# Kernel optimization log

Hardware: AMD Instinct MI355X
Metric: run time of the kernel (lower is better)

The kernel has to match this reference:

```python
import jax, jax.numpy as jnp
import numpy as np

B, M, A, NS, T = 256, 16, 4096, 1024, 64
DT = 0.001          # dt
DA = DT             # da == dt
REF_T = 0.004       # refractory period (s)
SYN_DELAY_BINS = 1  # floor(syn_delay / da)
N_NEUR = 500.0      # neurons per population (self.N)
A_GRID = jnp.linspace(0.0, A * DA, A + 1)[:-1]  # (A,) ages since last spike


def _get_plam(input_total, V_old, age, rp, amem, ft):
    # V_old: (B,M,K); input_total: (B,M,1); age broadcasts against (B,M,K)
    V_new = V_old + DA * (rp - V_old) * amem + DA * input_total
    V_new = jnp.where(age < REF_T, 0.0, V_new)
    lam = jnp.where(V_new == 0.0, 1e-8, jnp.exp(V_new - ft))  # firing intensity
    p = lam * DT
    Plam = jnp.where(p >= 0.01, 1.0 - jnp.exp(-p), p)
    return V_new, Plam, lam


def setup_inputs() -> dict:
    key = jax.random.key(0)
    ks = jax.random.split(key, 13)
    return {
        "x": jax.random.normal(ks[0], (B, M), jnp.float32),
        "V_t_old": jax.random.normal(ks[1], (B, M, A), jnp.float32),
        "logS_t_old": jax.random.normal(ks[2], (B, M, A), jnp.float32),
        "sampled_neuron_v": jax.random.normal(ks[3], (B, M, NS), jnp.float32),
        "sampled_neuron_lastfire": jax.random.uniform(ks[4], (B, M, NS), jnp.float32),
        "I_syn": jax.random.uniform(ks[5], (B, M, 1), jnp.float32),
        "amem": jax.random.uniform(ks[6], (M, 1), jnp.float32),
        "asyn": jax.random.uniform(ks[7], (M, 1), jnp.float32),
        "J": jax.random.normal(ks[8], (M, M), jnp.float32),
        "rp": jax.random.uniform(ks[9], (M, 1), jnp.float32),
        "ft": jax.random.uniform(ks[10], (M, 1), jnp.float32),
        "eps": jax.random.uniform(ks[11], (1,), jnp.float32),
        "Z_hist_est": jnp.clip(jax.random.uniform(ks[12], (B, M, A + T), jnp.float32), 1e-5, 1.0),
        "internal_clock": 32,
    }


def reference(x, V_t_old, logS_t_old, sampled_neuron_v, sampled_neuron_lastfire,
              I_syn, amem, asyn, J, rp, ft, eps, Z_hist_est, internal_clock):
    clk = int(internal_clock)
    # ---- synaptic current with exponential decay and delayed pop activity ----
    exp_syn = jnp.exp(-DT * asyn)  # (M,1)
    if clk > SYN_DELAY_BINS:
        Z_t_last = Z_hist_est[:, :, clk + A - SYN_DELAY_BINS - 1:clk + A - SYN_DELAY_BINS]
        I_syn = exp_syn * I_syn + (1.0 - exp_syn) * Z_t_last / DT
    # input_total: (B,M,1)
    input_total = jnp.einsum('bm,mn->bn', I_syn[:, :, 0], J)[:, :, None] + (x * eps)[:, :, None]

    # ---- population activity update ----
    Z_t = Z_hist_est[:, :, clk:clk + A][:, :, ::-1]          # (B,M,A), youngest age first
    Z_t_new = Z_hist_est[:, :, clk + A:clk + A + 1]          # (B,M,1)

    V_t_new, Plam, _ = _get_plam(input_total, V_t_old, A_GRID, rp, amem, ft)

    S_old = jnp.exp(logS_t_old)
    m_t = S_old * Z_t
    Zmacro = jnp.sum(m_t * Plam, axis=2, keepdims=True)
    mess = 1.0 - jnp.sum(m_t, axis=2, keepdims=True)
    v_t = (1.0 - S_old) * m_t
    num = jnp.sum(v_t * Plam, axis=2, keepdims=True)
    den = jnp.sum(v_t, axis=2, keepdims=True)
    lambda_t = jnp.where(den != 0.0, num / jnp.where(den == 0.0, 1.0, den), 0.0)  # nan -> 0
    Z = jnp.clip(Zmacro + lambda_t * mess, 0.0, 1.0)
    A_t = Z / DT
    var = Z / N_NEUR + 0.1 * DT / N_NEUR
    Z_nll = 0.5 * jnp.square(Z_t_new - Z) / var + 0.5 * jnp.log(var) + 0.5 * jnp.log(2.0 * 3.14)

    # ---- sampled-neuron spike likelihood ----
    snv_new, Plam_s, lam_s = _get_plam(input_total, sampled_neuron_v, sampled_neuron_lastfire, rp, amem, ft)
    ltdt = lam_s * DT
    lnPy = jnp.where(ltdt < 0.01, snv_new - ft + jnp.log(DT), jnp.log(Plam_s))
    lnP1_y = -ltdt

    return (A_t, Z, Z_nll, lnPy, lnP1_y, V_t_new, snv_new, I_syn)
```

## Files before the change

kernel.cpp:

```cpp
#include <hip/hip_runtime.h>

#define B_   256
#define M_   16
#define A_   4096
#define NS_  1024
#define T_   64
#define AT_  (A_ + T_)

static constexpr float DTc = 0.001f;
static constexpr float DAc = 0.001f;

static constexpr size_t OFF_AT    = 0;
static constexpr size_t OFF_Z     = 4096;
static constexpr size_t OFF_ZNLL  = 8192;
static constexpr size_t OFF_LNPY  = 12288;
static constexpr size_t OFF_LNP1Y = 12288 + 4194304;
static constexpr size_t OFF_VT    = 12288 + 2ull * 4194304;
static constexpr size_t OFF_SNV   = OFF_VT + 16777216ull;
static constexpr size_t OFF_ISYN  = OFF_SNV + 4194304ull;

__global__ __launch_bounds__(256) void lif_kernel(
    const float* __restrict__ x,
    const float* __restrict__ V_t_old,
    const float* __restrict__ logS_t_old,
    const float* __restrict__ snv_in,
    const float* __restrict__ snlf,
    const float* __restrict__ I_syn,
    const float* __restrict__ amem,
    const float* __restrict__ asyn,
    const float* __restrict__ J,
    const float* __restrict__ rp,
    const float* __restrict__ ft,
    const float* __restrict__ eps,
    const float* __restrict__ Z_hist,
    const int*   __restrict__ clk_ptr,
    float* __restrict__ out)
{
    const int row = blockIdx.x;
    const int b   = row >> 4;
    const int m   = row & 15;
    const int tid = threadIdx.x;

    __shared__ float sh_I[M_];
    __shared__ float sh_inT;
    __shared__ float sh_red[4][4];

    const int clk = *clk_ptr;

    if (tid < M_) {
        float es   = expf(-DTc * asyn[tid]);
        float Iold = I_syn[b * M_ + tid];
        float In   = Iold;
        if (clk > 1) {
            float zl = Z_hist[(size_t)(b * M_ + tid) * AT_ + (clk + A_ - 2)];
            In = es * Iold + (1.0f - es) * zl / DTc;
        }
        sh_I[tid] = In;
    }
    __syncthreads();
    if (tid == 0) {
        float dot = 0.0f;
#pragma unroll
        for (int mm = 0; mm < M_; ++mm) dot += sh_I[mm] * J[mm * M_ + m];
        sh_inT = dot + x[row] * eps[0];
        out[OFF_ISYN + row] = sh_I[m];
    }
    __syncthreads();

    const float a_m  = amem[m];
    const float rp_m = rp[m];
    const float ft_m = ft[m];
    const float inT  = sh_inT;

    const size_t rowA = (size_t)row * A_;
    const size_t rowZ = (size_t)row * AT_;

    float sZm = 0.0f, sM = 0.0f, sNum = 0.0f, sDen = 0.0f;

#pragma unroll
    for (int c = 0; c < 4; ++c) {
        const int a0 = c * 1024 + tid * 4;
        const float4 vo = *reinterpret_cast<const float4*>(V_t_old    + rowA + a0);
        const float4 ls = *reinterpret_cast<const float4*>(logS_t_old + rowA + a0);
        const float vov[4] = {vo.x, vo.y, vo.z, vo.w};
        const float lsv[4] = {ls.x, ls.y, ls.z, ls.w};
        const float* zp = Z_hist + rowZ + (clk + A_ - 1 - a0);
        float vres[4];
#pragma unroll
        for (int k = 0; k < 4; ++k) {
            const int a = a0 + k;
            float V = vov[k] + DAc * (rp_m - vov[k]) * a_m + DAc * inT;
            if (a < 4) V = 0.0f;
            float lam  = (V == 0.0f) ? 1e-8f : expf(V - ft_m);
            float p    = lam * DTc;
            float Plam = (p >= 0.01f) ? (1.0f - expf(-p)) : p;
            float S    = expf(lsv[k]);
            float z    = zp[-k];
            float mt   = S * z;
            sZm += mt * Plam;
            sM  += mt;
            float v = (1.0f - S) * mt;
            sNum += v * Plam;
            sDen += v;
            vres[k] = V;
        }
        *reinterpret_cast<float4*>(out + OFF_VT + rowA + a0) =
            make_float4(vres[0], vres[1], vres[2], vres[3]);
    }

    float vals[4] = {sZm, sM, sNum, sDen};
#pragma unroll
    for (int i = 0; i < 4; ++i) {
        float v = vals[i];
        for (int off = 32; off > 0; off >>= 1) v += __shfl_down(v, off, 64);
        vals[i] = v;
    }
    const int wave = tid >> 6, lane = tid & 63;
    if (lane == 0) {
#pragma unroll
        for (int i = 0; i < 4; ++i) sh_red[wave][i] = vals[i];
    }
    __syncthreads();
    if (tid == 0) {
        float Zm  = sh_red[0][0] + sh_red[1][0] + sh_red[2][0] + sh_red[3][0];
        float sMt = sh_red[0][1] + sh_red[1][1] + sh_red[2][1] + sh_red[3][1];
        float num = sh_red[0][2] + sh_red[1][2] + sh_red[2][2] + sh_red[3][2];
        float den = sh_red[0][3] + sh_red[1][3] + sh_red[2][3] + sh_red[3][3];
        float mess  = 1.0f - sMt;
        float lam_t = (den != 0.0f) ? (num / den) : 0.0f;
        float Z = Zm + lam_t * mess;
        Z = fminf(fmaxf(Z, 0.0f), 1.0f);
        float At  = Z / DTc;
        float var = Z / 500.0f + 0.1f * DTc / 500.0f;
        float ztn = Z_hist[rowZ + clk + A_];
        float d   = ztn - Z;
        float znll = 0.5f * (d * d) / var + 0.5f * logf(var) + 0.5f * logf(2.0f * 3.14f);
        out[OFF_AT   + row] = At;
        out[OFF_Z    + row] = Z;
        out[OFF_ZNLL + row] = znll;
    }

    {
        const size_t rowS = (size_t)row * NS_;
        const int s0 = tid * 4;
        const float4 v4  = *reinterpret_cast<const float4*>(snv_in + rowS + s0);
        const float4 lf4 = *reinterpret_cast<const float4*>(snlf   + rowS + s0);
        const float vv[4] = {v4.x, v4.y, v4.z, v4.w};
        const float lf[4] = {lf4.x, lf4.y, lf4.z, lf4.w};
        float vn[4], py[4], p1[4];
#pragma unroll
        for (int k = 0; k < 4; ++k) {
            float V = vv[k] + DAc * (rp_m - vv[k]) * a_m + DAc * inT;
            if (lf[k] < 0.004f) V = 0.0f;
            float lam  = (V == 0.0f) ? 1e-8f : expf(V - ft_m);
            float ltdt = lam * DTc;
            float Plam = (ltdt >= 0.01f) ? (1.0f - expf(-ltdt)) : ltdt;
            py[k] = (ltdt < 0.01f) ? (V - ft_m + logf(DTc)) : logf(Plam);
            p1[k] = -ltdt;
            vn[k] = V;
        }
        *reinterpret_cast<float4*>(out + OFF_SNV   + rowS + s0) = make_float4(vn[0], vn[1], vn[2], vn[3]);
        *reinterpret_cast<float4*>(out + OFF_LNPY  + rowS + s0) = make_float4(py[0], py[1], py[2], py[3]);
        *reinterpret_cast<float4*>(out + OFF_LNP1Y + rowS + s0) = make_float4(p1[0], p1[1], p1[2], p1[3]);
    }
}

extern "C" void kernel_launch(void* const* d_in, const int* in_sizes, int n_in,
                              void* d_out, int out_size, void* d_ws, size_t ws_size,
                              hipStream_t stream) {
    lif_kernel<<<B_ * M_, 256, 0, stream>>>(
        (const float*)d_in[0],
        (const float*)d_in[1],
        (const float*)d_in[2],
        (const float*)d_in[3],
        (const float*)d_in[4],
        (const float*)d_in[5],
        (const float*)d_in[6],
        (const float*)d_in[7],
        (const float*)d_in[8],
        (const float*)d_in[9],
        (const float*)d_in[10],
        (const float*)d_in[11],
        (const float*)d_in[12],
        (const int*)  d_in[13],
        (float*)d_out);
}
```

Before: 312.0 us.

## Hoist all global loads upfront and compute synaptic input via wave shuffles

All V, logS, Z-history and sampled-neuron loads are issued at the start, before the synaptic-input computation, and scheduling barriers keep them grouped so memory latency overlaps the dot product. The 16-element I_syn·J dot product now runs as a shuffle reduction inside each wavefront, which removes two block-wide __syncthreads and the shared-memory round trip. Z-history loads become reversed float4 loads when clk is aligned, the sampled-neuron work moves ahead of the final block reduction, and launch bounds request 4 blocks per CU. The cost is higher register pressure from holding many float4 values live at once, which could lower occupancy.

```diff
diff --git a/kernel.cpp b/kernel.cpp
--- a/kernel.cpp
+++ b/kernel.cpp
@@ -9,6 +9,7 @@
 
 static constexpr float DTc = 0.001f;
 static constexpr float DAc = 0.001f;
+static constexpr float LOG_DT = -6.907755278982137f;
 
 static constexpr size_t OFF_AT    = 0;
 static constexpr size_t OFF_Z     = 4096;
@@ -19,7 +20,11 @@
 static constexpr size_t OFF_SNV   = OFF_VT + 16777216ull;
 static constexpr size_t OFF_ISYN  = OFF_SNV + 4194304ull;
 
-__global__ __launch_bounds__(256) void lif_kernel(
+static __device__ __forceinline__ float4 ld4(const float* p) {
+    return *reinterpret_cast<const float4*>(p);
+}
+
+__global__ __launch_bounds__(256, 4) void lif_kernel(
     const float* __restrict__ x,
     const float* __restrict__ V_t_old,
     const float* __restrict__ logS_t_old,
@@ -36,116 +41,108 @@
     const int*   __restrict__ clk_ptr,
     float* __restrict__ out)
 {
-    const int row = blockIdx.x;
-    const int b   = row >> 4;
-    const int m   = row & 15;
-    const int tid = threadIdx.x;
-
-    __shared__ float sh_I[M_];
-    __shared__ float sh_inT;
+    const int row  = blockIdx.x;
+    const int b    = row >> 4;
+    const int m    = row & 15;
+    const int tid  = threadIdx.x;
+    const int lane = tid & 63;
+
     __shared__ float sh_red[4][4];
 
-    const int clk = *clk_ptr;
-
-    if (tid < M_) {
-        float es   = expf(-DTc * asyn[tid]);
-        float Iold = I_syn[b * M_ + tid];
-        float In   = Iold;
-        if (clk > 1) {
-            float zl = Z_hist[(size_t)(b * M_ + tid) * AT_ + (clk + A_ - 2)];
-            In = es * Iold + (1.0f - es) * zl / DTc;
-        }
-        sh_I[tid] = In;
-    }
-    __syncthreads();
-    if (tid == 0) {
-        float dot = 0.0f;
-#pragma unroll
-        for (int mm = 0; mm < M_; ++mm) dot += sh_I[mm] * J[mm * M_ + m];
-        sh_inT = dot + x[row] * eps[0];
-        out[OFF_ISYN + row] = sh_I[m];
-    }
-    __syncthreads();
-
+    const size_t rowA = (size_t)row * A_;
+    const size_t rowS = (size_t)row * NS_;
+
+    const int   clk  = *clk_ptr;
+    const float xv   = x[row];
+    const float ev   = eps[0];
     const float a_m  = amem[m];
     const float rp_m = rp[m];
     const float ft_m = ft[m];
-    const float inT  = sh_inT;
-
-    const size_t rowA = (size_t)row * A_;
+
     const size_t rowZ = (size_t)row * AT_;
-
-    float sZm = 0.0f, sM = 0.0f, sNum = 0.0f, sDen = 0.0f;
-
-#pragma unroll
-    for (int c = 0; c < 4; ++c) {
-        const int a0 = c * 1024 + tid * 4;
-        const float4 vo = *reinterpret_cast<const float4*>(V_t_old    + rowA + a0);
-        const float4 ls = *reinterpret_cast<const float4*>(logS_t_old + rowA + a0);
-        const float vov[4] = {vo.x, vo.y, vo.z, vo.w};
-        const float lsv[4] = {ls.x, ls.y, ls.z, ls.w};
-        const float* zp = Z_hist + rowZ + (clk + A_ - 1 - a0);
-        float vres[4];
-#pragma unroll
-        for (int k = 0; k < 4; ++k) {
-            const int a = a0 + k;
-            float V = vov[k] + DAc * (rp_m - vov[k]) * a_m + DAc * inT;
-            if (a < 4) V = 0.0f;
-            float lam  = (V == 0.0f) ? 1e-8f : expf(V - ft_m);
-            float p    = lam * DTc;
-            float Plam = (p >= 0.01f) ? (1.0f - expf(-p)) : p;
-            float S    = expf(lsv[k]);
-            float z    = zp[-k];
-            float mt   = S * z;
-            sZm += mt * Plam;
-            sM  += mt;
-            float v = (1.0f - S) * mt;
-            sNum += v * Plam;
-            sDen += v;
-            vres[k] = V;
-        }
-        *reinterpret_cast<float4*>(out + OFF_VT + rowA + a0) =
-            make_float4(vres[0], vres[1], vres[2], vres[3]);
-    }
-
-    float vals[4] = {sZm, sM, sNum, sDen};
-#pragma unroll
-    for (int i = 0; i < 4; ++i) {
-        float v = vals[i];
-        for (int off = 32; off > 0; off >>= 1) v += __shfl_down(v, off, 64);
-        vals[i] = v;
-    }
-    const int wave = tid >> 6, lane = tid & 63;
-    if (lane == 0) {
-#pragma unroll
-        for (int i = 0; i < 4; ++i) sh_red[wave][i] = vals[i];
-    }
-    __syncthreads();
-    if (tid == 0) {
-        float Zm  = sh_red[0][0] + sh_red[1][0] + sh_red[2][0] + sh_red[3][0];
-        float sMt = sh_red[0][1] + sh_red[1][1] + sh_red[2][1] + sh_red[3][1];
-        float num = sh_red[0][2] + sh_red[1][2] + sh_red[2][2] + sh_red[3][2];
-        float den = sh_red[0][3] + sh_red[1][3] + sh_red[2][3] + sh_red[3][3];
-        float mess  = 1.0f - sMt;
-        float lam_t = (den != 0.0f) ? (num / den) : 0.0f;
-        float Z = Zm + lam_t * mess;
-        Z = fminf(fmaxf(Z, 0.0f), 1.0f);
-        float At  = Z / DTc;
-        float var = Z / 500.0f + 0.1f * DTc / 500.0f;
-        float ztn = Z_hist[rowZ + clk + A_];
-        float d   = ztn - Z;
-        float znll = 0.5f * (d * d) / var + 0.5f * logf(var) + 0.5f * logf(2.0f * 3.14f);
-        out[OFF_AT   + row] = At;
-        out[OFF_Z    + row] = Z;
-        out[OFF_ZNLL + row] = znll;
-    }
+    const float  ztn  = Z_hist[rowZ + clk + A_];
+
+    float asy = 0.0f, Iold = 0.0f, Jv = 0.0f, zl = 0.0f;
+    if (lane < M_) {
+        asy  = asyn[lane];
+        Iold = I_syn[b * M_ + lane];
+        Jv   = J[lane * M_ + m];
+        if (clk > 1) zl = Z_hist[(size_t)(b * M_ + lane) * AT_ + (clk + A_ - 2)];
+    }
+    __builtin_amdgcn_sched_barrier(0);
+
+    const float* pV = V_t_old    + rowA + tid * 4;
+    const float* pS = logS_t_old + rowA + tid * 4;
+    const float4 vA = ld4(pV);          const float4 vB = ld4(pV + 1024);
+    const float4 vC = ld4(pV + 2048);   const float4 vD = ld4(pV + 3072);
+    const float4 sA = ld4(pS);          const float4 sB = ld4(pS + 1024);
+    const float4 sC = ld4(pS + 2048);   const float4 sD = ld4(pS + 3072);
+    const float4 n4  = ld4(snv_in + rowS + tid * 4);
+    const float4 lf4 = ld4(snlf   + rowS + tid * 4);
+
+    const bool  zal = ((clk & 3) == 0);
+    const float* pZ = Z_hist + rowZ + (clk + A_ - 4 - tid * 4);
+    float4 zA, zB, zC, zD;
+    if (zal) {
+        zA = ld4(pZ);          zB = ld4(pZ - 1024);
+        zC = ld4(pZ - 2048);   zD = ld4(pZ - 3072);
+    } else {
+        zA = make_float4(pZ[0], pZ[1], pZ[2], pZ[3]);
+        zB = make_float4(pZ[-1024], pZ[-1023], pZ[-1022], pZ[-1021]);
+        zC = make_float4(pZ[-2048], pZ[-2047], pZ[-2046], pZ[-2045]);
+        zD = make_float4(pZ[-3072], pZ[-3071], pZ[-3070], pZ[-3069]);
+    }
+    __builtin_amdgcn_sched_barrier(0);
+
+    float In = Iold;
+    if (clk > 1 && lane < M_) {
+        const float es = expf(-DTc * asy);
+        In = es * Iold + (1.0f - es) * zl / DTc;
+    }
+    if (tid == m) out[OFF_ISYN + row] = In;
+    float t = (lane < M_) ? In * Jv : 0.0f;
+#pragma unroll
+    for (int off = 8; off > 0; off >>= 1) t += __shfl_xor(t, off, 16);
+    const float inT = __shfl(t, 0, 64) + xv * ev;
+
+    float sZm = 0.0f, sMt = 0.0f, sNum = 0.0f, sDen = 0.0f;
+
+#define CHUNK(cidx, vc, sc, zc)                                                 \
+    do {                                                                        \
+        const int a0 = (cidx) * 1024 + tid * 4;                                 \
+        const float vov[4]  = {vc.x, vc.y, vc.z, vc.w};                         \
+        const float lsv[4]  = {sc.x, sc.y, sc.z, sc.w};                         \
+        const float zrev[4] = {zc.w, zc.z, zc.y, zc.x};                         \
+        float vres[4];                                                          \
+        _Pragma("unroll")                                                       \
+        for (int k = 0; k < 4; ++k) {                                           \
+            const int a = a0 + k;                                               \
+            float V = vov[k] + DAc * (rp_m - vov[k]) * a_m + DAc * inT;         \
+            if (a < 4) V = 0.0f;                               \
+            float lam  = (V == 0.0f) ? 1e-8f : expf(V - ft_m);                  \
+            float p    = lam * DTc;                                             \
+            float Plam = (p >= 0.01f) ? (1.0f - expf(-p)) : p;                  \
+            float S    = expf(lsv[k]);                                          \
+            float mt   = S * zrev[k];                                           \
+            sZm += mt * Plam;                                                   \
+            sMt += mt;                                                          \
+            float v = (1.0f - S) * mt;                                          \
+            sNum += v * Plam;                                                   \
+            sDen += v;                                                          \
+            vres[k] = V;                                                        \
+        }                                                                       \
+        *reinterpret_cast<float4*>(out + OFF_VT + rowA + a0) =                  \
+            make_float4(vres[0], vres[1], vres[2], vres[3]);                    \
+    } while (0)
+
+    CHUNK(0, vA, sA, zA);
+    CHUNK(1, vB, sB, zB);
+    CHUNK(2, vC, sC, zC);
+    CHUNK(3, vD, sD, zD);
+#undef CHUNK
 
     {
-        const size_t rowS = (size_t)row * NS_;
-        const int s0 = tid * 4;
-        const float4 v4  = *reinterpret_cast<const float4*>(snv_in + rowS + s0);
-        const float4 lf4 = *reinterpret_cast<const float4*>(snlf   + rowS + s0);
-        const float vv[4] = {v4.x, v4.y, v4.z, v4.w};
+        const float vv[4] = {n4.x, n4.y, n4.z, n4.w};
         const float lf[4] = {lf4.x, lf4.y, lf4.z, lf4.w};
         float vn[4], py[4], p1[4];
 #pragma unroll
@@ -155,13 +152,45 @@
             float lam  = (V == 0.0f) ? 1e-8f : expf(V - ft_m);
             float ltdt = lam * DTc;
             float Plam = (ltdt >= 0.01f) ? (1.0f - expf(-ltdt)) : ltdt;
-            py[k] = (ltdt < 0.01f) ? (V - ft_m + logf(DTc)) : logf(Plam);
+            py[k] = (ltdt < 0.01f) ? (V - ft_m + LOG_DT) : logf(Plam);
             p1[k] = -ltdt;
             vn[k] = V;
         }
+        const int s0 = tid * 4;
         *reinterpret_cast<float4*>(out + OFF_SNV   + rowS + s0) = make_float4(vn[0], vn[1], vn[2], vn[3]);
         *reinterpret_cast<float4*>(out + OFF_LNPY  + rowS + s0) = make_float4(py[0], py[1], py[2], py[3]);
         *reinterpret_cast<float4*>(out + OFF_LNP1Y + rowS + s0) = make_float4(p1[0], p1[1], p1[2], p1[3]);
+    }
+
+    float vals[4] = {sZm, sMt, sNum, sDen};
+#pragma unroll
+    for (int i = 0; i < 4; ++i) {
+        float v = vals[i];
+        for (int off = 32; off > 0; off >>= 1) v += __shfl_down(v, off, 64);
+        vals[i] = v;
+    }
+    const int wave = tid >> 6;
+    if (lane == 0) {
+#pragma unroll
+        for (int i = 0; i < 4; ++i) sh_red[wave][i] = vals[i];
+    }
+    __syncthreads();
+    if (tid == 0) {
+        float Zm  = sh_red[0][0] + sh_red[1][0] + sh_red[2][0] + sh_red[3][0];
+        float sM  = sh_red[0][1] + sh_red[1][1] + sh_red[2][1] + sh_red[3][1];
+        float num = sh_red[0][2] + sh_red[1][2] + sh_red[2][2] + sh_red[3][2];
+        float den = sh_red[0][3] + sh_red[1][3] + sh_red[2][3] + sh_red[3][3];
+        float mess  = 1.0f - sM;
+        float lam_t = (den != 0.0f) ? (num / den) : 0.0f;
+        float Z = Zm + lam_t * mess;
+        Z = fminf(fmaxf(Z, 0.0f), 1.0f);
+        float At  = Z / DTc;
+        float var = Z / 500.0f + 0.1f * DTc / 500.0f;
+        float d   = ztn - Z;
+        float znll = 0.5f * (d * d) / var + 0.5f * logf(var) + 0.5f * logf(2.0f * 3.14f);
+        out[OFF_AT   + row] = At;
+        out[OFF_Z    + row] = Z;
+        out[OFF_ZNLL + row] = znll;
     }
 }
 
```

New measurement: 307.4 us. Within noise of the previous version (-1.5%).
